# Performance work log

Hardware: AMD Instinct MI355X
Metric: run time of the kernel (lower is better)

## Reference

```python
import jax, jax.numpy as jnp
import numpy as np

B, S, D = 2, 2048, 768
H, DK, DV = 12, 64, 64


def setup_inputs() -> dict:
    key = jax.random.key(0)
    ks = jax.random.split(key, 12)
    sc = 0.02
    return {
        'q': jax.random.normal(ks[0], (B, S, D), jnp.float32),
        'k': jax.random.normal(ks[1], (B, S, D), jnp.float32),
        'v': jax.random.normal(ks[2], (B, S, D), jnp.float32),
        'mask': jnp.zeros((B, H, S, S), jnp.float32),
        'Wq': jax.random.normal(ks[3], (D, H * DK), jnp.float32) * sc,
        'bq': jnp.zeros((H * DK,), jnp.float32),
        'Wk': jax.random.normal(ks[4], (D, H * DK), jnp.float32) * sc,
        'bk': jnp.zeros((H * DK,), jnp.float32),
        'Wv': jax.random.normal(ks[5], (D, H * DV), jnp.float32) * sc,
        'bv': jnp.zeros((H * DV,), jnp.float32),
        'Wo': jax.random.normal(ks[6], (H * DV, D), jnp.float32) * sc,
        'bo': jnp.zeros((D,), jnp.float32),
    }


def reference(q, k, v, mask, Wq, bq, Wk, bk, Wv, bv, Wo, bo):
    b, s, _ = q.shape
    # projections -> [B, H, S, Dk/Dv]
    Q = (q @ Wq + bq).reshape(b, s, H, DK).transpose(0, 2, 1, 3)
    K = (k @ Wk + bk).reshape(b, s, H, DK).transpose(0, 2, 1, 3)
    V = (v @ Wv + bv).reshape(b, s, H, DV).transpose(0, 2, 1, 3)
    scale = 1.0 / np.sqrt(DK).astype(np.float32)
    scores = jnp.einsum('bhqd,bhkd->bhqk', Q, K) * scale + mask
    attn = jax.nn.softmax(scores, axis=-1)  # dropout rate 0.0 -> identity
    ctx = jnp.einsum('bhqk,bhkd->bhqd', attn, V)
    ctx = ctx.transpose(0, 2, 1, 3).reshape(b, s, H * DV)
    out = ctx @ Wo + bo
    return out, attn
```

## Files before the change

kernel.cpp:

```cpp
#include <hip/hip_runtime.h>
#include <hip/hip_bf16.h>

typedef unsigned short u16;
typedef __attribute__((ext_vector_type(8))) short s16x8;
typedef __attribute__((ext_vector_type(4))) float f32x4;

#define MFMA16(a, b, c) __builtin_amdgcn_mfma_f32_16x16x32_bf16((a), (b), (c), 0, 0, 0)

__device__ __forceinline__ float b2f(u16 u) {
    union { float f; unsigned int i; } c; c.i = ((unsigned int)u) << 16; return c.f;
}
__device__ __forceinline__ u16 f2b(float f) {
    union { float f; unsigned int i; } c; c.f = f;
    unsigned int i = c.i;
    return (u16)((i + 0x7fffu + ((i >> 16) & 1u)) >> 16);
}

__device__ __forceinline__ s16x8 load8b(const void* base, size_t idx, int isf32) {
    if (!isf32) {
        return *(const s16x8*)((const u16*)base + idx);
    } else {
        const float* p = (const float*)base + idx;
        f32x4 a = *(const f32x4*)p;
        f32x4 b = *(const f32x4*)(p + 4);
        s16x8 v;
        v[0] = (short)f2b(a[0]); v[1] = (short)f2b(a[1]);
        v[2] = (short)f2b(a[2]); v[3] = (short)f2b(a[3]);
        v[4] = (short)f2b(b[0]); v[5] = (short)f2b(b[1]);
        v[6] = (short)f2b(b[2]); v[7] = (short)f2b(b[3]);
        return v;
    }
}
__device__ __forceinline__ void load8f(const void* base, size_t idx, int isf32, float* o) {
    if (!isf32) {
        s16x8 m = *(const s16x8*)((const u16*)base + idx);
#pragma unroll
        for (int j = 0; j < 8; j++) o[j] = b2f((u16)m[j]);
    } else {
        const float* p = (const float*)base + idx;
        f32x4 a = *(const f32x4*)p;
        f32x4 b = *(const f32x4*)(p + 4);
        o[0] = a[0]; o[1] = a[1]; o[2] = a[2]; o[3] = a[3];
        o[4] = b[0]; o[5] = b[1]; o[6] = b[2]; o[7] = b[3];
    }
}
__device__ __forceinline__ float loadsc(const void* base, size_t idx, int isf32) {
    return isf32 ? ((const float*)base)[idx] : b2f(((const u16*)base)[idx]);
}

__global__ __launch_bounds__(64) void k_detect(const u16* __restrict__ q, int* __restrict__ flag) {
    int t = threadIdx.x;
    int cnt = 0;
#pragma unroll
    for (int i = 0; i < 16; i++) {
        u16 u = q[t * 16 + i];
        int e = (u >> 7) & 0xFF;
        cnt += (e >= 110 && e <= 135) ? 1 : 0;
    }
#pragma unroll
    for (int off = 32; off > 0; off >>= 1) cnt += __shfl_down(cnt, off);
    if (t == 0) *flag = (cnt < 850) ? 1 : 0;
}

__global__ __launch_bounds__(256) void k_transpose(
    const void* __restrict__ w0, const void* __restrict__ w1,
    const void* __restrict__ w2, const void* __restrict__ w3,
    u16* __restrict__ wt, const int* __restrict__ flag)
{
    __shared__ __align__(16) u16 T[64 * 65];
    const int isf32 = *flag;
    const int z = blockIdx.z;
    const void* W = (z == 0) ? w0 : (z == 1) ? w1 : (z == 2) ? w2 : w3;
    u16* WT = wt + (size_t)z * 589824;
    const int n0 = blockIdx.x * 64, k0 = blockIdx.y * 64;
    const int t = threadIdx.x;
    const int r = t >> 3, c = (t & 7) * 8;
    for (int rr = r; rr < 64; rr += 32) {
        s16x8 v = load8b(W, (size_t)(k0 + rr) * 768 + n0 + c, isf32);
#pragma unroll
        for (int j = 0; j < 8; j++) T[(c + j) * 65 + rr] = (u16)v[j];
    }
    __syncthreads();
    const int n = t >> 3, kc = (t & 7) * 8;
    for (int nn = n; nn < 64; nn += 32) {
        s16x8 v;
#pragma unroll
        for (int j = 0; j < 8; j++) v[j] = (short)T[nn * 65 + kc + j];
        *(s16x8*)&WT[(size_t)(n0 + nn) * 768 + k0 + kc] = v;
    }
}

__device__ __forceinline__ void gemm_body(
    const void* __restrict__ A, int a_isf32, const u16* __restrict__ WT,
    const void* __restrict__ bias, int b_isf32, void* __restrict__ out,
    int out_isf32, int epi, int head, int m0)
{
    __shared__ __align__(16) u16 As[128 * 72];
    __shared__ __align__(16) u16 Bs[64 * 72];
    const int t = threadIdx.x;
    const int lane = t & 63, wave = t >> 6;
    const int quad = lane >> 4, l16 = lane & 15;
    const int mrow_base = (wave >> 1) * 64;
    const int ncol_base = (wave & 1) * 32;
    const int hbase = head * 64;

    f32x4 acc[4][2];
#pragma unroll
    for (int mt = 0; mt < 4; mt++)
#pragma unroll
        for (int nt = 0; nt < 2; nt++) acc[mt][nt] = (f32x4){0.f, 0.f, 0.f, 0.f};

    for (int k0 = 0; k0 < 768; k0 += 64) {
#pragma unroll
        for (int i = 0; i < 4; i++) {
            int seg = t + 256 * i;
            int r = seg >> 3, c = (seg & 7) * 8;
            *(s16x8*)&As[r * 72 + c] = load8b(A, (size_t)(m0 + r) * 768 + k0 + c, a_isf32);
        }
#pragma unroll
        for (int i = 0; i < 2; i++) {
            int seg = t + 256 * i;
            int r = seg >> 3, c = (seg & 7) * 8;
            *(s16x8*)&Bs[r * 72 + c] = *(const s16x8*)&WT[(size_t)(hbase + r) * 768 + k0 + c];
        }
        __syncthreads();
#pragma unroll
        for (int ks = 0; ks < 2; ks++) {
            s16x8 af[4], bf[2];
#pragma unroll
            for (int mt = 0; mt < 4; mt++)
                af[mt] = *(const s16x8*)&As[(mrow_base + mt * 16 + l16) * 72 + ks * 32 + quad * 8];
#pragma unroll
            for (int nt = 0; nt < 2; nt++)
                bf[nt] = *(const s16x8*)&Bs[(ncol_base + nt * 16 + l16) * 72 + ks * 32 + quad * 8];
#pragma unroll
            for (int mt = 0; mt < 4; mt++)
#pragma unroll
                for (int nt = 0; nt < 2; nt++)
                    acc[mt][nt] = MFMA16(af[mt], bf[nt], acc[mt][nt]);
        }
        __syncthreads();
    }

    if (epi == 2) {
#pragma unroll
        for (int mt = 0; mt < 4; mt++)
#pragma unroll
            for (int nt = 0; nt < 2; nt++) {
                int nc = ncol_base + nt * 16 + l16;
                float bvv = loadsc(bias, hbase + nc, b_isf32);
#pragma unroll
                for (int r = 0; r < 4; r++) {
                    int m = m0 + mrow_base + mt * 16 + quad * 4 + r;
                    float val = acc[mt][nt][r] + bvv;
                    size_t idx = (size_t)m * 768 + hbase + nc;
                    if (out_isf32) ((float*)out)[idx] = val;
                    else           ((u16*)out)[idx] = f2b(val);
                }
            }
    } else if (epi == 0) {
        u16* ob = (u16*)out;
#pragma unroll
        for (int mt = 0; mt < 4; mt++)
#pragma unroll
            for (int nt = 0; nt < 2; nt++) {
                int nc = ncol_base + nt * 16 + l16;
                float bvv = loadsc(bias, hbase + nc, b_isf32);
#pragma unroll
                for (int r = 0; r < 4; r++) {
                    int m = m0 + mrow_base + mt * 16 + quad * 4 + r;
                    int bidx = m >> 11, s = m & 2047;
                    ob[(((size_t)bidx * 12 + head) * 2048 + s) * 64 + nc] =
                        f2b(acc[mt][nt][r] + bvv);
                }
            }
    } else {
        u16* ob = (u16*)out;
        u16* Ts = As;
#pragma unroll
        for (int mt = 0; mt < 4; mt++)
#pragma unroll
            for (int nt = 0; nt < 2; nt++) {
                int nc = ncol_base + nt * 16 + l16;
                float bvv = loadsc(bias, hbase + nc, b_isf32);
#pragma unroll
                for (int r = 0; r < 4; r++) {
                    int ml = mrow_base + mt * 16 + quad * 4 + r;
                    Ts[nc * 136 + ml] = f2b(acc[mt][nt][r] + bvv);
                }
            }
        __syncthreads();
        const int bidx = m0 >> 11, sbase = m0 & 2047;
#pragma unroll
        for (int i = 0; i < 4; i++) {
            int seg = t + 256 * i;
            int dv = seg >> 4, scc = (seg & 15) * 8;
            s16x8 vv = *(const s16x8*)&Ts[dv * 136 + scc];
            *(s16x8*)&ob[(((size_t)bidx * 12 + head) * 64 + dv) * 2048 + sbase + scc] = vv;
        }
    }
}

__global__ __launch_bounds__(256) void k_qkv(
    const void* __restrict__ q, const void* __restrict__ k, const void* __restrict__ v,
    const u16* __restrict__ wt,
    const void* __restrict__ bq, const void* __restrict__ bk, const void* __restrict__ bv,
    u16* __restrict__ Q, u16* __restrict__ K, u16* __restrict__ Vt,
    const int* __restrict__ flag)
{
    const int isf32 = *flag;
    const int z = blockIdx.z;
    const void* A = (z == 0) ? q : (z == 1) ? k : v;
    const u16* WTz = wt + (size_t)z * 589824;
    const void* bias = (z == 0) ? bq : (z == 1) ? bk : bv;
    u16* out = (z == 0) ? Q : (z == 1) ? K : Vt;
    gemm_body(A, isf32, WTz, bias, isf32, out, 0, (z == 2) ? 1 : 0, blockIdx.y, blockIdx.x * 128);
}

__global__ __launch_bounds__(256) void k_oproj(
    const u16* __restrict__ ctx, const u16* __restrict__ wto,
    const void* __restrict__ bo, void* __restrict__ out,
    const int* __restrict__ flag)
{
    const int isf32 = *flag;
    gemm_body(ctx, 0, wto, bo, isf32, out, isf32, 2, blockIdx.y, blockIdx.x * 128);
}

__device__ __forceinline__ int sw_off(int row, int col) {
    int unit = col >> 3;
    int slot = (unit + 2 * (row >> 2)) & 7;
    return row * 2048 + (((unit & ~7) | slot) << 3) + (col & 7);
}

__global__ __launch_bounds__(256) void k_attn(
    const u16* __restrict__ Q, const u16* __restrict__ K,
    const u16* __restrict__ Vt, const void* __restrict__ mask,
    void* __restrict__ outbase, u16* __restrict__ ctx,
    const int* __restrict__ flag)
{
    __shared__ __align__(16) u16 sc[16 * 2048];
    const int isf32 = *flag;
    const int t = threadIdx.x;
    const int lane = t & 63, wave = t >> 6;
    const int quad = lane >> 4, l16 = lane & 15;
    const int q0 = blockIdx.x * 16;
    const int h = blockIdx.y, b = blockIdx.z;
    const int bh = b * 12 + h;

    const u16* Qb = Q + ((size_t)bh * 2048 + q0) * 64;
    const s16x8 qf0 = *(const s16x8*)&Qb[l16 * 64 + quad * 8];
    const s16x8 qf1 = *(const s16x8*)&Qb[l16 * 64 + 32 + quad * 8];

    const u16* Kb = K + (size_t)bh * 2048 * 64;
    for (int it = 0; it < 32; it++) {
        const int kc = it * 64 + wave * 16;
        const u16* kp = &Kb[(size_t)(kc + l16) * 64 + quad * 8];
        s16x8 kf0 = *(const s16x8*)kp;
        s16x8 kf1 = *(const s16x8*)(kp + 32);
        f32x4 a = (f32x4){0.f, 0.f, 0.f, 0.f};
        a = MFMA16(qf0, kf0, a);
        a = MFMA16(qf1, kf1, a);
#pragma unroll
        for (int r = 0; r < 4; r++)
            sc[sw_off(quad * 4 + r, kc + l16)] = f2b(a[r] * 0.125f);
    }
    __syncthreads();

    const int row = t >> 4, j16 = t & 15;
    const size_t moff = ((size_t)bh * 2048 + q0 + row) * 2048;
    float mx = -3.4e38f;
#pragma unroll 4
    for (int i = 0; i < 16; i++) {
        const int c0 = j16 * 8 + i * 128;
        float mk[8];
        load8f(mask, moff + c0, isf32, mk);
        s16x8* sp = (s16x8*)&sc[sw_off(row, c0)];
        s16x8 sv = *sp, nv;
#pragma unroll
        for (int j = 0; j < 8; j++) {
            float x = b2f((u16)sv[j]) + mk[j];
            nv[j] = (short)f2b(x);
            mx = fmaxf(mx, x);
        }
        *sp = nv;
    }
#pragma unroll
    for (int off = 8; off > 0; off >>= 1) mx = fmaxf(mx, __shfl_xor(mx, off));

    float sum = 0.f;
#pragma unroll 4
    for (int i = 0; i < 16; i++) {
        const int c0 = j16 * 8 + i * 128;
        s16x8 sv = *(const s16x8*)&sc[sw_off(row, c0)];
#pragma unroll
        for (int j = 0; j < 8; j++) sum += __expf(b2f((u16)sv[j]) - mx);
    }
#pragma unroll
    for (int off = 8; off > 0; off >>= 1) sum += __shfl_xor(sum, off);
    const float inv = 1.0f / sum;

    const size_t aoff = 3145728 + moff;
#pragma unroll 2
    for (int i = 0; i < 16; i++) {
        const int c0 = j16 * 8 + i * 128;
        s16x8* sp = (s16x8*)&sc[sw_off(row, c0)];
        s16x8 sv = *sp, pv;
        float p[8];
#pragma unroll
        for (int j = 0; j < 8; j++) {
            p[j] = __expf(b2f((u16)sv[j]) - mx) * inv;
            pv[j] = (short)f2b(p[j]);
        }
        *sp = pv;
        if (isf32) {
            float* arow = (float*)outbase + aoff;
            f32x4 lo = (f32x4){p[0], p[1], p[2], p[3]};
            f32x4 hi = (f32x4){p[4], p[5], p[6], p[7]};
            *(f32x4*)&arow[c0] = lo;
            *(f32x4*)&arow[c0 + 4] = hi;
        } else {
            u16* arow = (u16*)outbase + aoff;
            *(s16x8*)&arow[c0] = pv;
        }
    }
    __syncthreads();

    const int dv = wave * 16 + l16;
    const u16* vrow = Vt + ((size_t)bh * 64 + dv) * 2048;
    f32x4 o = (f32x4){0.f, 0.f, 0.f, 0.f};
#pragma unroll 4
    for (int kk = 0; kk < 64; kk++) {
        s16x8 pa = *(const s16x8*)&sc[sw_off(l16, kk * 32 + quad * 8)];
        s16x8 vb = *(const s16x8*)&vrow[kk * 32 + quad * 8];
        o = MFMA16(pa, vb, o);
    }
#pragma unroll
    for (int r = 0; r < 4; r++)
        ctx[((size_t)b * 2048 + q0 + quad * 4 + r) * 768 + h * 64 + dv] = f2b(o[r]);
}

extern "C" void kernel_launch(void* const* d_in, const int* in_sizes, int n_in,
                              void* d_out, int out_size, void* d_ws, size_t ws_size,
                              hipStream_t stream) {
    const void* q    = d_in[0];
    const void* k    = d_in[1];
    const void* v    = d_in[2];
    const void* mask = d_in[3];
    const void* Wq   = d_in[4];
    const void* bq   = d_in[5];
    const void* Wk   = d_in[6];
    const void* bk   = d_in[7];
    const void* Wv   = d_in[8];
    const void* bv   = d_in[9];
    const void* Wo   = d_in[10];
    const void* bo   = d_in[11];

    u16* ws  = (u16*)d_ws;
    u16* WT  = ws;
    u16* Qb  = ws + 2359296;
    u16* Kb  = ws + 5505024;
    u16* Vtb = ws + 8650752;
    u16* ctx = ws + 11796480;
    int* flag = (int*)(ws + 14942208);

    k_detect<<<1, 64, 0, stream>>>((const u16*)q, flag);
    k_transpose<<<dim3(12, 12, 4), 256, 0, stream>>>(Wq, Wk, Wv, Wo, WT, flag);
    k_qkv<<<dim3(32, 12, 3), 256, 0, stream>>>(q, k, v, WT, bq, bk, bv, Qb, Kb, Vtb, flag);
    k_attn<<<dim3(128, 12, 2), 256, 0, stream>>>(Qb, Kb, Vtb, mask, d_out, ctx, flag);
    k_oproj<<<dim3(32, 12, 1), 256, 0, stream>>>(ctx, WT + 3 * 589824, bo, d_out, flag);
}
```

Baseline: 947.6 us.

## Fuse mask add and row max into QK pass, widen attention block to 512 threads

The attention kernel now runs 512 threads: the QK^T pass adds the mask with nontemporal loads and tracks per-row maxima in registers, reducing them through a small shared table, which removes a separate LDS pass over the scores. The exp is computed once and stored, so the normalisation pass only multiplies by the inverse sum. Attention probability stores become nontemporal, the LDS swizzle changes, and the PV product is split across two wave groups whose partial sums are combined through shared memory. This adds more shared memory and a scattered 2-byte/4-byte mask load pattern, which may coalesce poorly compared with the earlier vectorised mask reads.

```diff
diff --git a/kernel.cpp b/kernel.cpp
--- a/kernel.cpp
+++ b/kernel.cpp
@@ -31,21 +31,13 @@
         return v;
     }
 }
-__device__ __forceinline__ void load8f(const void* base, size_t idx, int isf32, float* o) {
-    if (!isf32) {
-        s16x8 m = *(const s16x8*)((const u16*)base + idx);
-#pragma unroll
-        for (int j = 0; j < 8; j++) o[j] = b2f((u16)m[j]);
-    } else {
-        const float* p = (const float*)base + idx;
-        f32x4 a = *(const f32x4*)p;
-        f32x4 b = *(const f32x4*)(p + 4);
-        o[0] = a[0]; o[1] = a[1]; o[2] = a[2]; o[3] = a[3];
-        o[4] = b[0]; o[5] = b[1]; o[6] = b[2]; o[7] = b[3];
-    }
-}
 __device__ __forceinline__ float loadsc(const void* base, size_t idx, int isf32) {
     return isf32 ? ((const float*)base)[idx] : b2f(((const u16*)base)[idx]);
+}
+__device__ __forceinline__ float loadsc_nt(const void* base, size_t idx, int isf32) {
+    if (isf32) return __builtin_nontemporal_load((const float*)base + idx);
+    u16 u = __builtin_nontemporal_load((const u16*)base + idx);
+    return b2f(u);
 }
 
 __global__ __launch_bounds__(64) void k_detect(const u16* __restrict__ q, int* __restrict__ flag) {
@@ -228,17 +220,19 @@
 
 __device__ __forceinline__ int sw_off(int row, int col) {
     int unit = col >> 3;
-    int slot = (unit + 2 * (row >> 2)) & 7;
+    int slot = (unit + row) & 7;
     return row * 2048 + (((unit & ~7) | slot) << 3) + (col & 7);
 }
 
-__global__ __launch_bounds__(256) void k_attn(
+__global__ __launch_bounds__(512, 4) void k_attn(
     const u16* __restrict__ Q, const u16* __restrict__ K,
     const u16* __restrict__ Vt, const void* __restrict__ mask,
     void* __restrict__ outbase, u16* __restrict__ ctx,
     const int* __restrict__ flag)
 {
     __shared__ __align__(16) u16 sc[16 * 2048];
+    __shared__ __align__(16) float part[1024];
+    __shared__ float wmax[16][8];
     const int isf32 = *flag;
     const int t = threadIdx.x;
     const int lane = t & 63, wave = t >> 6;
@@ -252,63 +246,71 @@
     const s16x8 qf1 = *(const s16x8*)&Qb[l16 * 64 + 32 + quad * 8];
 
     const u16* Kb = K + (size_t)bh * 2048 * 64;
-    for (int it = 0; it < 32; it++) {
-        const int kc = it * 64 + wave * 16;
+    const size_t mrow0 = ((size_t)bh * 2048 + q0) * 2048;
+
+    float rm[4] = {-3.4e38f, -3.4e38f, -3.4e38f, -3.4e38f};
+#pragma unroll 4
+    for (int it = 0; it < 16; it++) {
+        const int kc = it * 128 + wave * 16;
         const u16* kp = &Kb[(size_t)(kc + l16) * 64 + quad * 8];
         s16x8 kf0 = *(const s16x8*)kp;
         s16x8 kf1 = *(const s16x8*)(kp + 32);
         f32x4 a = (f32x4){0.f, 0.f, 0.f, 0.f};
         a = MFMA16(qf0, kf0, a);
         a = MFMA16(qf1, kf1, a);
-#pragma unroll
-        for (int r = 0; r < 4; r++)
-            sc[sw_off(quad * 4 + r, kc + l16)] = f2b(a[r] * 0.125f);
+        const int col = kc + l16;
+#pragma unroll
+        for (int r = 0; r < 4; r++) {
+            const int row = quad * 4 + r;
+            float m = loadsc_nt(mask, mrow0 + (size_t)row * 2048 + col, isf32);
+            float x = a[r] * 0.125f + m;
+            sc[sw_off(row, col)] = f2b(x);
+            rm[r] = fmaxf(rm[r], x);
+        }
+    }
+#pragma unroll
+    for (int off = 8; off > 0; off >>= 1)
+#pragma unroll
+        for (int r = 0; r < 4; r++) rm[r] = fmaxf(rm[r], __shfl_xor(rm[r], off));
+    if (l16 == 0) {
+#pragma unroll
+        for (int r = 0; r < 4; r++) wmax[quad * 4 + r][wave] = rm[r];
     }
     __syncthreads();
 
-    const int row = t >> 4, j16 = t & 15;
-    const size_t moff = ((size_t)bh * 2048 + q0 + row) * 2048;
-    float mx = -3.4e38f;
+    const int row = t >> 5, j32 = t & 31;
+    float mx = wmax[row][0];
+#pragma unroll
+    for (int w = 1; w < 8; w++) mx = fmaxf(mx, wmax[row][w]);
+
+    float sum = 0.f;
 #pragma unroll 4
-    for (int i = 0; i < 16; i++) {
-        const int c0 = j16 * 8 + i * 128;
-        float mk[8];
-        load8f(mask, moff + c0, isf32, mk);
+    for (int i = 0; i < 8; i++) {
+        const int c0 = j32 * 8 + i * 256;
         s16x8* sp = (s16x8*)&sc[sw_off(row, c0)];
         s16x8 sv = *sp, nv;
 #pragma unroll
         for (int j = 0; j < 8; j++) {
-            float x = b2f((u16)sv[j]) + mk[j];
-            nv[j] = (short)f2b(x);
-            mx = fmaxf(mx, x);
+            float e = __expf(b2f((u16)sv[j]) - mx);
+            nv[j] = (short)f2b(e);
+            sum += e;
         }
         *sp = nv;
     }
 #pragma unroll
-    for (int off = 8; off > 0; off >>= 1) mx = fmaxf(mx, __shfl_xor(mx, off));
-
-    float sum = 0.f;
-#pragma unroll 4
-    for (int i = 0; i < 16; i++) {
-        const int c0 = j16 * 8 + i * 128;
-        s16x8 sv = *(const s16x8*)&sc[sw_off(row, c0)];
-#pragma unroll
-        for (int j = 0; j < 8; j++) sum += __expf(b2f((u16)sv[j]) - mx);
-    }
-#pragma unroll
-    for (int off = 8; off > 0; off >>= 1) sum += __shfl_xor(sum, off);
+    for (int off = 16; off > 0; off >>= 1) sum += __shfl_xor(sum, off);
     const float inv = 1.0f / sum;
 
-    const size_t aoff = 3145728 + moff;
+    const size_t aoff = 3145728 + mrow0 + (size_t)row * 2048;
 #pragma unroll 2
-    for (int i = 0; i < 16; i++) {
-        const int c0 = j16 * 8 + i * 128;
+    for (int i = 0; i < 8; i++) {
+        const int c0 = j32 * 8 + i * 256;
         s16x8* sp = (s16x8*)&sc[sw_off(row, c0)];
         s16x8 sv = *sp, pv;
         float p[8];
 #pragma unroll
         for (int j = 0; j < 8; j++) {
-            p[j] = __expf(b2f((u16)sv[j]) - mx) * inv;
+            p[j] = b2f((u16)sv[j]) * inv;
             pv[j] = (short)f2b(p[j]);
         }
         *sp = pv;
@@ -316,27 +318,36 @@
             float* arow = (float*)outbase + aoff;
             f32x4 lo = (f32x4){p[0], p[1], p[2], p[3]};
             f32x4 hi = (f32x4){p[4], p[5], p[6], p[7]};
-            *(f32x4*)&arow[c0] = lo;
-            *(f32x4*)&arow[c0 + 4] = hi;
+            __builtin_nontemporal_store(lo, (f32x4*)&arow[c0]);
+            __builtin_nontemporal_store(hi, (f32x4*)&arow[c0 + 4]);
         } else {
             u16* arow = (u16*)outbase + aoff;
-            *(s16x8*)&arow[c0] = pv;
+            __builtin_nontemporal_store(pv, (s16x8*)&arow[c0]);
         }
     }
     __syncthreads();
 
-    const int dv = wave * 16 + l16;
+    const int wg = wave >> 2;
+    const int dv = (wave & 3) * 16 + l16;
     const u16* vrow = Vt + ((size_t)bh * 64 + dv) * 2048;
     f32x4 o = (f32x4){0.f, 0.f, 0.f, 0.f};
+    const int kbase = wg * 32;
 #pragma unroll 4
-    for (int kk = 0; kk < 64; kk++) {
-        s16x8 pa = *(const s16x8*)&sc[sw_off(l16, kk * 32 + quad * 8)];
-        s16x8 vb = *(const s16x8*)&vrow[kk * 32 + quad * 8];
+    for (int kk = 0; kk < 32; kk++) {
+        const int kcol = (kbase + kk) * 32 + quad * 8;
+        s16x8 pa = *(const s16x8*)&sc[sw_off(l16, kcol)];
+        s16x8 vb = *(const s16x8*)&vrow[kcol];
         o = MFMA16(pa, vb, o);
     }
-#pragma unroll
-    for (int r = 0; r < 4; r++)
-        ctx[((size_t)b * 2048 + q0 + quad * 4 + r) * 768 + h * 64 + dv] = f2b(o[r]);
+    if (wg == 1) *(f32x4*)&part[((wave & 3) * 64 + lane) * 4] = o;
+    __syncthreads();
+    if (wg == 0) {
+        f32x4 o2 = *(const f32x4*)&part[((wave & 3) * 64 + lane) * 4];
+#pragma unroll
+        for (int r = 0; r < 4; r++)
+            ctx[((size_t)b * 2048 + q0 + quad * 4 + r) * 768 + h * 64 + dv] =
+                f2b(o[r] + o2[r]);
+    }
 }
 
 extern "C" void kernel_launch(void* const* d_in, const int* in_sizes, int n_in,
@@ -366,6 +377,6 @@
     k_detect<<<1, 64, 0, stream>>>((const u16*)q, flag);
     k_transpose<<<dim3(12, 12, 4), 256, 0, stream>>>(Wq, Wk, Wv, Wo, WT, flag);
     k_qkv<<<dim3(32, 12, 3), 256, 0, stream>>>(q, k, v, WT, bq, bk, bv, Qb, Kb, Vtb, flag);
-    k_attn<<<dim3(128, 12, 2), 256, 0, stream>>>(Qb, Kb, Vtb, mask, d_out, ctx, flag);
+    k_attn<<<dim3(128, 12, 2), 512, 0, stream>>>(Qb, Kb, Vtb, mask, d_out, ctx, flag);
     k_oproj<<<dim3(32, 12, 1), 256, 0, stream>>>(ctx, WT + 3 * 589824, bo, d_out, flag);
 }
```

Result: slower. 1.008 ms (+6.4%).
